# Performance work log

Measured on AMD Instinct MI355X. Metric: run time of the kernel, lower is better.

Reference implementation:

```python
import jax, jax.numpy as jnp
import numpy as np

B, S, D = 16384, 2048, 512

def mish(z):
    # z * tanh(softplus(z))
    return z * jnp.tanh(jax.nn.softplus(z))

def setup_inputs() -> dict:
    key = jax.random.key(0)
    ks = jax.random.split(key, 8)
    sc_d = 1.0 / np.sqrt(D)
    sc_s = 1.0 / np.sqrt(S)
    return {
        "x": jax.random.normal(ks[0], (B, D), jnp.float32),
        "samples": jax.random.normal(ks[1], (S, D), jnp.float32),
        "W1": jax.random.normal(ks[2], (D, D), jnp.float32) * sc_d,
        "b1": jax.random.normal(ks[3], (D,), jnp.float32) * sc_d,
        "W2": jax.random.normal(ks[4], (D, D), jnp.float32) * sc_d,
        "b2": jax.random.normal(ks[5], (D,), jnp.float32) * sc_d,
        "Wn1": jax.random.normal(ks[6], (S, S), jnp.float32) * sc_s,
        "Wn2": jax.random.normal(ks[7], (S, S), jnp.float32) * sc_s,
    }

def reference(x, samples, W1, b1, W2, b2, Wn1, Wn2):
    def dml(t):
        h = mish(t @ W1.T + b1)
        return h @ W2.T + b2

    # forward: x -> dml -> rbf kernel vs dml(samples) -> nystrom MLP
    x_dml = dml(x)            # [B, D]
    sam_new = dml(samples)    # [S, D]

    # fused batched cdist (Euclidean, not squared) + RBF
    d2 = (jnp.sum(x_dml * x_dml, axis=-1, keepdims=True)
          + jnp.sum(sam_new * sam_new, axis=-1)[None, :]
          - 2.0 * (x_dml @ sam_new.T))
    dist = jnp.sqrt(jnp.maximum(d2, 0.0))
    K = jnp.exp(-dist)        # [B, S] == exp(-||xi - sam_j||_2)

    # nystrom MLP (no bias)
    h = mish(K @ Wn1.T)
    return h @ Wn2.T          # [B, S]
```

## Files before the change

kernel.cpp:

```cpp
#include <hip/hip_runtime.h>
#include <cstdint>
#include <cstddef>

#define B_ROWS 16384
#define S_ROWS 2048
#define D_DIM  512

typedef __attribute__((ext_vector_type(8))) short          s16x8;
typedef __attribute__((ext_vector_type(8))) unsigned short u16x8;
typedef __attribute__((ext_vector_type(4))) float          f32x4;

static __device__ __forceinline__ unsigned short f2bf(float f) {
  unsigned int u = __builtin_bit_cast(unsigned int, f);
  u = (u + 0x7FFFu + ((u >> 16) & 1u)) >> 16;
  return (unsigned short)u;
}
static __device__ __forceinline__ float bf2f(unsigned short h) {
  unsigned int u = ((unsigned int)h) << 16;
  return __builtin_bit_cast(float, u);
}
static __device__ __forceinline__ float mish_f(float z) {
  float sp = (z > 20.0f) ? z : log1pf(expf(z));
  return z * tanhf(sp);
}

static __device__ __forceinline__ f32x4 mfma16(s16x8 a, s16x8 b, f32x4 c) {
  return __builtin_amdgcn_mfma_f32_16x16x32_bf16(a, b, c, 0, 0, 0);
}

static __device__ __forceinline__ void gload16(unsigned short* lds_dst,
                                               const unsigned short* g_src) {
  __builtin_amdgcn_global_load_lds(
      (const __attribute__((address_space(1))) unsigned int*)g_src,
      (__attribute__((address_space(3))) unsigned int*)lds_dst,
      16, 0, 0);
}

__global__ void split_kernel(const float* __restrict__ in,
                             unsigned short* __restrict__ hi,
                             unsigned short* __restrict__ lo, int n4) {
  const int stride = gridDim.x * blockDim.x;
  for (int i = blockIdx.x * blockDim.x + threadIdx.x; i < n4; i += stride) {
    const float4 v = ((const float4*)in)[i];
    float f[4] = {v.x, v.y, v.z, v.w};
    unsigned short hh[4], ll[4];
#pragma unroll
    for (int j = 0; j < 4; ++j) {
      hh[j] = f2bf(f[j]);
      ll[j] = f2bf(f[j] - bf2f(hh[j]));
    }
    ((ushort4*)hi)[i] = make_ushort4(hh[0], hh[1], hh[2], hh[3]);
    ((ushort4*)lo)[i] = make_ushort4(ll[0], ll[1], ll[2], ll[3]);
  }
}

__global__ void norm_kernel(const unsigned short* __restrict__ hi,
                            const unsigned short* __restrict__ lo,
                            float* __restrict__ out, int rows) {
  const int gw = (int)((blockIdx.x * blockDim.x + threadIdx.x) >> 6);
  const int l  = threadIdx.x & 63;
  if (gw >= rows) return;
  const size_t base = (size_t)gw * D_DIM + (size_t)l * 8;
  const u16x8 h8 = *(const u16x8*)(hi + base);
  const u16x8 l8 = *(const u16x8*)(lo + base);
  float s = 0.f;
#pragma unroll
  for (int j = 0; j < 8; ++j) {
    float v = bf2f(h8[j]) + bf2f(l8[j]);
    s += v * v;
  }
#pragma unroll
  for (int m = 32; m; m >>= 1) s += __shfl_xor(s, m, 64);
  if (l == 0) out[gw] = s;
}

#define BKT 32

template <int EPI>
__global__ __launch_bounds__(256) void gemm_split(
    const unsigned short* __restrict__ Ahi, const unsigned short* __restrict__ Alo,
    const unsigned short* __restrict__ Bhi, const unsigned short* __restrict__ Blo,
    const float* __restrict__ bias, const float* __restrict__ nrmA,
    const float* __restrict__ nrmB,
    unsigned short* __restrict__ Chi, unsigned short* __restrict__ Clo,
    float* __restrict__ Cf, int M, int N, int K) {
  __shared__ __align__(16) unsigned short lds[4 * 128 * BKT];
  unsigned short* tAh = lds;
  unsigned short* tAl = lds + 128 * BKT;
  unsigned short* tBh = lds + 2 * 128 * BKT;
  unsigned short* tBl = lds + 3 * 128 * BKT;

  const int tid = threadIdx.x;
  const int w = tid >> 6;
  const int l = tid & 63;
  const int nTm = M >> 7;
  const int tm = (int)(blockIdx.x) % nTm;
  const int tn = (int)(blockIdx.x) / nTm;
  const int rowA0 = tm << 7;
  const int rowB0 = tn << 7;

  const int wm = w >> 1, wn = w & 1;
  const int fr = l & 15, fg = l >> 4;

  f32x4 acc[4][4];
#pragma unroll
  for (int i = 0; i < 4; ++i)
#pragma unroll
    for (int j = 0; j < 4; ++j) acc[i][j] = (f32x4){0.f, 0.f, 0.f, 0.f};

  const int srow   = l >> 2;
  const int gchunk = (l & 3) ^ (srow & 3);

  const int nk = K >> 5;
  for (int kt = 0; kt < nk; ++kt) {
    const int k0 = kt << 5;
#pragma unroll
    for (int j = 0; j < 2; ++j) {
      const int rl = w * 32 + j * 16;
      const int gr = rl + srow;
      const size_t ga = (size_t)(rowA0 + gr) * (size_t)K + (size_t)(k0 + gchunk * 8);
      const size_t gb = (size_t)(rowB0 + gr) * (size_t)K + (size_t)(k0 + gchunk * 8);
      gload16(tAh + rl * BKT, Ahi + ga);
      gload16(tAl + rl * BKT, Alo + ga);
      gload16(tBh + rl * BKT, Bhi + gb);
      gload16(tBl + rl * BKT, Blo + gb);
    }
    __syncthreads();

    s16x8 ah[4], al[4], bh[4], bl[4];
#pragma unroll
    for (int mi = 0; mi < 4; ++mi) {
      const int r = wm * 64 + mi * 16 + fr;
      const int c = (fg ^ (r & 3)) << 3;
      ah[mi] = *(const s16x8*)&tAh[r * BKT + c];
      al[mi] = *(const s16x8*)&tAl[r * BKT + c];
    }
#pragma unroll
    for (int ni = 0; ni < 4; ++ni) {
      const int r = wn * 64 + ni * 16 + fr;
      const int c = (fg ^ (r & 3)) << 3;
      bh[ni] = *(const s16x8*)&tBh[r * BKT + c];
      bl[ni] = *(const s16x8*)&tBl[r * BKT + c];
    }
#pragma unroll
    for (int mi = 0; mi < 4; ++mi)
#pragma unroll
      for (int ni = 0; ni < 4; ++ni) {
        acc[mi][ni] = mfma16(al[mi], bh[ni], acc[mi][ni]);
        acc[mi][ni] = mfma16(ah[mi], bl[ni], acc[mi][ni]);
        acc[mi][ni] = mfma16(ah[mi], bh[ni], acc[mi][ni]);
      }
    __syncthreads();
  }

  const int rowBase = rowA0 + wm * 64;
  const int colBase = rowB0 + wn * 64;
#pragma unroll
  for (int mi = 0; mi < 4; ++mi) {
#pragma unroll
    for (int ni = 0; ni < 4; ++ni) {
      const int col = colBase + ni * 16 + fr;
      float badd = 0.f;
      if constexpr (EPI == 0 || EPI == 1) badd = bias[col];
      float nB = 0.f;
      if constexpr (EPI == 2) nB = nrmB[col];
#pragma unroll
      for (int r = 0; r < 4; ++r) {
        const int row = rowBase + mi * 16 + fg * 4 + r;
        float v = acc[mi][ni][r];
        if constexpr (EPI == 0 || EPI == 1) v += badd;
        if constexpr (EPI == 2) {
          float d2 = nrmA[row] + nB - 2.f * v;
          v = expf(-sqrtf(fmaxf(d2, 0.f)));
        }
        if constexpr (EPI == 0 || EPI == 3) v = mish_f(v);
        const size_t o = (size_t)row * (size_t)N + (size_t)col;
        if constexpr (EPI == 4) {
          Cf[o] = v;
        } else {
          unsigned short h = f2bf(v);
          Chi[o] = h;
          Clo[o] = f2bf(v - bf2f(h));
        }
      }
    }
  }
}

template <int EPI>
static void launch_gemm(const unsigned short* Ahi, const unsigned short* Alo,
                        const unsigned short* Bhi, const unsigned short* Blo,
                        const float* bias, const float* nrmA, const float* nrmB,
                        unsigned short* Chi, unsigned short* Clo, float* Cf,
                        int M, int N, int K, hipStream_t stream) {
  dim3 grid((unsigned)((M >> 7) * (N >> 7)));
  gemm_split<EPI><<<grid, dim3(256), 0, stream>>>(Ahi, Alo, Bhi, Blo, bias,
                                                  nrmA, nrmB, Chi, Clo, Cf, M, N, K);
}

static int grid_for(int n4) {
  int g = (n4 + 255) / 256;
  return g > 4096 ? 4096 : g;
}

extern "C" void kernel_launch(void* const* d_in, const int* in_sizes, int n_in,
                              void* d_out, int out_size, void* d_ws, size_t ws_size,
                              hipStream_t stream) {
  const float* x       = (const float*)d_in[0];
  const float* samples = (const float*)d_in[1];
  const float* W1      = (const float*)d_in[2];
  const float* b1      = (const float*)d_in[3];
  const float* W2      = (const float*)d_in[4];
  const float* b2      = (const float*)d_in[5];
  const float* Wn1     = (const float*)d_in[6];
  const float* Wn2     = (const float*)d_in[7];
  float* outF = (float*)d_out;

  if (ws_size < 167845888ull) return;

  char* ob = (char*)d_out;
  unsigned short* xhi  = (unsigned short*)(ob + 0);
  unsigned short* xlo  = (unsigned short*)(ob + 16777216);
  unsigned short* t1hi = (unsigned short*)(ob + 33554432);
  unsigned short* t1lo = (unsigned short*)(ob + 50331648);
  unsigned short* t2hi = (unsigned short*)(ob + 67108864);
  unsigned short* t2lo = (unsigned short*)(ob + 69206016);
  unsigned short* Khi  = (unsigned short*)(ob + 0);
  unsigned short* Klo  = (unsigned short*)(ob + 67108864);

  char* wb = (char*)d_ws;
  unsigned short* hhi  = (unsigned short*)(wb + 0);
  unsigned short* hlo  = (unsigned short*)(wb + 67108864);
  unsigned short* xdhi = (unsigned short*)(wb + 0);
  unsigned short* xdlo = (unsigned short*)(wb + 16777216);
  unsigned short* snhi = (unsigned short*)(wb + 33554432);
  unsigned short* snlo = (unsigned short*)(wb + 35651584);
  unsigned short* samhi= (unsigned short*)(wb + 37748736);
  unsigned short* samlo= (unsigned short*)(wb + 39845888);
  unsigned short* W1hi = (unsigned short*)(wb + 41943040);
  unsigned short* W1lo = (unsigned short*)(wb + 42467328);
  unsigned short* W2hi = (unsigned short*)(wb + 42991616);
  unsigned short* W2lo = (unsigned short*)(wb + 43515904);
  unsigned short* Wn1hi= (unsigned short*)(wb + 134217728);
  unsigned short* Wn1lo= (unsigned short*)(wb + 142606336);
  unsigned short* Wn2hi= (unsigned short*)(wb + 150994944);
  unsigned short* Wn2lo= (unsigned short*)(wb + 159383552);
  float* nx            = (float*)(wb + 167772160);
  float* ns            = (float*)(wb + 167837696);

  const dim3 tpb(256);

  {
    int n4;
    n4 = B_ROWS * D_DIM / 4;
    split_kernel<<<grid_for(n4), tpb, 0, stream>>>(x, xhi, xlo, n4);
    n4 = S_ROWS * D_DIM / 4;
    split_kernel<<<grid_for(n4), tpb, 0, stream>>>(samples, samhi, samlo, n4);
    n4 = D_DIM * D_DIM / 4;
    split_kernel<<<grid_for(n4), tpb, 0, stream>>>(W1, W1hi, W1lo, n4);
    split_kernel<<<grid_for(n4), tpb, 0, stream>>>(W2, W2hi, W2lo, n4);
    n4 = S_ROWS * S_ROWS / 4;
    split_kernel<<<grid_for(n4), tpb, 0, stream>>>(Wn1, Wn1hi, Wn1lo, n4);
    split_kernel<<<grid_for(n4), tpb, 0, stream>>>(Wn2, Wn2hi, Wn2lo, n4);
  }

  launch_gemm<0>(xhi, xlo, W1hi, W1lo, b1, nullptr, nullptr, t1hi, t1lo, nullptr,
                 B_ROWS, D_DIM, D_DIM, stream);
  launch_gemm<1>(t1hi, t1lo, W2hi, W2lo, b2, nullptr, nullptr, xdhi, xdlo, nullptr,
                 B_ROWS, D_DIM, D_DIM, stream);
  launch_gemm<0>(samhi, samlo, W1hi, W1lo, b1, nullptr, nullptr, t2hi, t2lo, nullptr,
                 S_ROWS, D_DIM, D_DIM, stream);
  launch_gemm<1>(t2hi, t2lo, W2hi, W2lo, b2, nullptr, nullptr, snhi, snlo, nullptr,
                 S_ROWS, D_DIM, D_DIM, stream);

  norm_kernel<<<dim3(B_ROWS / 4), tpb, 0, stream>>>(xdhi, xdlo, nx, B_ROWS);
  norm_kernel<<<dim3(S_ROWS / 4), tpb, 0, stream>>>(snhi, snlo, ns, S_ROWS);

  launch_gemm<2>(xdhi, xdlo, snhi, snlo, nullptr, nx, ns, Khi, Klo, nullptr,
                 B_ROWS, S_ROWS, D_DIM, stream);

  launch_gemm<3>(Khi, Klo, Wn1hi, Wn1lo, nullptr, nullptr, nullptr, hhi, hlo, nullptr,
                 B_ROWS, S_ROWS, S_ROWS, stream);

  launch_gemm<4>(hhi, hlo, Wn2hi, Wn2lo, nullptr, nullptr, nullptr, nullptr, nullptr,
                 outF, B_ROWS, S_ROWS, S_ROWS, stream);
}
```

Before: 1.497 ms.

## Interleave hi/lo tiles in LDS with XOR swizzle and XCD-aware block remap

Merges the separate hi and lo LDS tiles into one 128-byte row per matrix row, with an 8-way XOR swizzle so each lane's global load fills either the hi or the lo half. The fragment reads become byte-offset loads where the lo half sits at offset XOR 64. Source and destination pointers are now computed once outside the k-loop. Block indices are remapped so consecutive tiles land on the same XCD, and tile order switches to row-major over N, which is meant to improve L2 reuse. Together these aim to cut LDS bank conflicts, address arithmetic and cross-XCD cache misses, at the cost of more complex index math.

```diff
diff --git a/kernel.cpp b/kernel.cpp
--- a/kernel.cpp
+++ b/kernel.cpp
@@ -74,7 +74,6 @@
   if (l == 0) out[gw] = s;
 }
 
-#define BKT 32
 
 template <int EPI>
 __global__ __launch_bounds__(256) void gemm_split(
@@ -84,18 +83,23 @@
     const float* __restrict__ nrmB,
     unsigned short* __restrict__ Chi, unsigned short* __restrict__ Clo,
     float* __restrict__ Cf, int M, int N, int K) {
-  __shared__ __align__(16) unsigned short lds[4 * 128 * BKT];
-  unsigned short* tAh = lds;
-  unsigned short* tAl = lds + 128 * BKT;
-  unsigned short* tBh = lds + 2 * 128 * BKT;
-  unsigned short* tBl = lds + 3 * 128 * BKT;
+  __shared__ __align__(16) unsigned short lds[2 * 128 * 64];
+  unsigned short* tA = lds;
+  unsigned short* tB = lds + 128 * 64;
 
   const int tid = threadIdx.x;
   const int w = tid >> 6;
   const int l = tid & 63;
-  const int nTm = M >> 7;
-  const int tm = (int)(blockIdx.x) % nTm;
-  const int tn = (int)(blockIdx.x) / nTm;
+
+  const int nwg = (int)gridDim.x;
+  {
+  }
+  const int q8 = nwg >> 3, r8 = nwg & 7;
+  const int xcd = (int)blockIdx.x & 7, boff = (int)blockIdx.x >> 3;
+  const int swz = (xcd < r8 ? xcd * (q8 + 1) : r8 * (q8 + 1) + (xcd - r8) * q8) + boff;
+  const int nTn = N >> 7;
+  const int tm = swz / nTn;
+  const int tn = swz - tm * nTn;
   const int rowA0 = tm << 7;
   const int rowB0 = tn << 7;
 
@@ -108,39 +112,52 @@
 #pragma unroll
     for (int j = 0; j < 4; ++j) acc[i][j] = (f32x4){0.f, 0.f, 0.f, 0.f};
 
-  const int srow   = l >> 2;
-  const int gchunk = (l & 3) ^ (srow & 3);
+  const int pos   = l & 7;
+  const int rsub  = (l >> 3) & 7;
+  const int c     = pos ^ rsub;
+  const bool isHi = (c < 4);
+  const int celem = (c & 3) << 3;
+
+  const unsigned short* srcA[4];
+  const unsigned short* srcB[4];
+  unsigned short* dstA[4];
+  unsigned short* dstB[4];
+#pragma unroll
+  for (int j = 0; j < 4; ++j) {
+    const int rl = w * 32 + j * 8;
+    const int gr = rl + (l >> 3);
+    srcA[j] = (isHi ? Ahi : Alo) + (size_t)(rowA0 + gr) * (size_t)K + celem;
+    srcB[j] = (isHi ? Bhi : Blo) + (size_t)(rowB0 + gr) * (size_t)K + celem;
+    dstA[j] = tA + rl * 64;
+    dstB[j] = tB + rl * 64;
+  }
+
+  const int pbyte = (fg ^ (fr & 7)) << 4;
+  const char* tAc = (const char*)tA;
+  const char* tBc = (const char*)tB;
 
   const int nk = K >> 5;
   for (int kt = 0; kt < nk; ++kt) {
     const int k0 = kt << 5;
 #pragma unroll
-    for (int j = 0; j < 2; ++j) {
-      const int rl = w * 32 + j * 16;
-      const int gr = rl + srow;
-      const size_t ga = (size_t)(rowA0 + gr) * (size_t)K + (size_t)(k0 + gchunk * 8);
-      const size_t gb = (size_t)(rowB0 + gr) * (size_t)K + (size_t)(k0 + gchunk * 8);
-      gload16(tAh + rl * BKT, Ahi + ga);
-      gload16(tAl + rl * BKT, Alo + ga);
-      gload16(tBh + rl * BKT, Bhi + gb);
-      gload16(tBl + rl * BKT, Blo + gb);
+    for (int j = 0; j < 4; ++j) {
+      gload16(dstA[j], srcA[j] + k0);
+      gload16(dstB[j], srcB[j] + k0);
     }
     __syncthreads();
 
     s16x8 ah[4], al[4], bh[4], bl[4];
 #pragma unroll
     for (int mi = 0; mi < 4; ++mi) {
-      const int r = wm * 64 + mi * 16 + fr;
-      const int c = (fg ^ (r & 3)) << 3;
-      ah[mi] = *(const s16x8*)&tAh[r * BKT + c];
-      al[mi] = *(const s16x8*)&tAl[r * BKT + c];
+      const int base = ((wm << 6) + (mi << 4) + fr) << 7;
+      ah[mi] = *(const s16x8*)(tAc + (base + pbyte));
+      al[mi] = *(const s16x8*)(tAc + ((base + pbyte) ^ 64));
     }
 #pragma unroll
     for (int ni = 0; ni < 4; ++ni) {
-      const int r = wn * 64 + ni * 16 + fr;
-      const int c = (fg ^ (r & 3)) << 3;
-      bh[ni] = *(const s16x8*)&tBh[r * BKT + c];
-      bl[ni] = *(const s16x8*)&tBl[r * BKT + c];
+      const int base = ((wn << 6) + (ni << 4) + fr) << 7;
+      bh[ni] = *(const s16x8*)(tBc + (base + pbyte));
+      bl[ni] = *(const s16x8*)(tBc + ((base + pbyte) ^ 64));
     }
 #pragma unroll
     for (int mi = 0; mi < 4; ++mi)
```

Measured after the change: 1.475 ms. Within noise of the previous version (-1.5%).

## Rewrite split-bf16 GEMM as 256x256 tile, 4-stage pipelined, XCD-swizzled kernel

Applied to the files above, without the earlier changes.

Replaces the 128x128, 256-thread GEMM with a 256x256 tile over 512 threads. It streams the three split-bf16 products (hi*hi, hi*lo, lo*hi) as consecutive K passes through a 4-slot LDS ring, with explicit vmcnt waits and raw barriers so global loads overlap MFMA work. It also adds XCD-aware block remapping, a new LDS swizzle, and s_setprio around the MFMA block. The goal is to hide global-load latency, raise data reuse per tile and improve L2 locality, at the cost of a large register footprint (8x4 accumulators), 128KB of LDS per block, and hand-counted waitcnt logic that is fragile.

```diff
diff --git a/kernel.cpp b/kernel.cpp
--- a/kernel.cpp
+++ b/kernel.cpp
@@ -74,89 +74,117 @@
   if (l == 0) out[gw] = s;
 }
 
-#define BKT 32
-
 template <int EPI>
-__global__ __launch_bounds__(256) void gemm_split(
+__global__ __launch_bounds__(512, 2) void gemm8(
     const unsigned short* __restrict__ Ahi, const unsigned short* __restrict__ Alo,
     const unsigned short* __restrict__ Bhi, const unsigned short* __restrict__ Blo,
     const float* __restrict__ bias, const float* __restrict__ nrmA,
     const float* __restrict__ nrmB,
     unsigned short* __restrict__ Chi, unsigned short* __restrict__ Clo,
     float* __restrict__ Cf, int M, int N, int K) {
-  __shared__ __align__(16) unsigned short lds[4 * 128 * BKT];
-  unsigned short* tAh = lds;
-  unsigned short* tAl = lds + 128 * BKT;
-  unsigned short* tBh = lds + 2 * 128 * BKT;
-  unsigned short* tBl = lds + 3 * 128 * BKT;
+  __shared__ __align__(16) unsigned short lds[4 * 16384];
 
   const int tid = threadIdx.x;
-  const int w = tid >> 6;
-  const int l = tid & 63;
-  const int nTm = M >> 7;
-  const int tm = (int)(blockIdx.x) % nTm;
-  const int tn = (int)(blockIdx.x) / nTm;
-  const int rowA0 = tm << 7;
-  const int rowB0 = tn << 7;
-
-  const int wm = w >> 1, wn = w & 1;
+  const int w = tid >> 6, l = tid & 63;
+  const int wm = w >> 2, wn = w & 3;
   const int fr = l & 15, fg = l >> 4;
 
-  f32x4 acc[4][4];
-#pragma unroll
-  for (int i = 0; i < 4; ++i)
+  const int nwg = (int)gridDim.x;
+  const int q8 = nwg >> 3, r8 = nwg & 7;
+  const int xcd = (int)blockIdx.x & 7, boff = (int)blockIdx.x >> 3;
+  const int swz = (xcd < r8 ? xcd * (q8 + 1) : r8 * (q8 + 1) + (xcd - r8) * q8) + boff;
+  const int nTn = N >> 8;
+  const int tm = swz / nTn, tn = swz - tm * nTn;
+  const int rowA0 = tm << 8, rowB0 = tn << 8;
+
+  int rE[2], kcE[2];
+#pragma unroll
+  for (int e = 0; e < 2; ++e) {
+    const int d = tid + e * 512;
+    const int pr = d >> 3;
+    const int c8 = (d & 7) ^ (pr & 7);
+    rE[e]  = (pr << 1) | (c8 >> 2);
+    kcE[e] = (c8 & 3) << 3;
+  }
+  size_t gofA0 = (size_t)(rowA0 + rE[0]) * (size_t)K + kcE[0];
+  size_t gofA1 = (size_t)(rowA0 + rE[1]) * (size_t)K + kcE[1];
+  size_t gofB0 = (size_t)(rowB0 + rE[0]) * (size_t)K + kcE[0];
+  size_t gofB1 = (size_t)(rowB0 + rE[1]) * (size_t)K + kcE[1];
+  const int wof = w << 9;
+
+  int iss_slot = 0, iss_k = 0, iss_pass = 0;
+  const unsigned short* pA = Ahi;
+  const unsigned short* pB = Bhi;
+
+#define ISSUE_UNIT()                                                     \
+  do {                                                                   \
+    unsigned short* sb = lds + (iss_slot << 14);                         \
+    gload16(sb + wof,          pA + iss_k + gofA0);                      \
+    gload16(sb + 4096 + wof,   pA + iss_k + gofA1);                      \
+    gload16(sb + 8192 + wof,   pB + iss_k + gofB0);                      \
+    gload16(sb + 12288 + wof,  pB + iss_k + gofB1);                      \
+    iss_slot = (iss_slot + 1) & 3;                                       \
+    iss_k += 32;                                                         \
+    if (iss_k == K) {                                                    \
+      iss_k = 0; ++iss_pass;                                             \
+      pA = (iss_pass == 2) ? Alo : Ahi;                                  \
+      pB = (iss_pass == 1) ? Blo : Bhi;                                  \
+    }                                                                    \
+  } while (0)
+
+  const int frh = fr >> 1;
+  const int p = (((fr & 1) << 2) | fg) ^ (frh & 7);
+  const int aab = ((wm << 6) + frh) * 128 + p * 16;
+  const int bbb = 16384 + ((wn << 5) + frh) * 128 + p * 16;
+
+  f32x4 acc[8][4];
+#pragma unroll
+  for (int i = 0; i < 8; ++i)
 #pragma unroll
     for (int j = 0; j < 4; ++j) acc[i][j] = (f32x4){0.f, 0.f, 0.f, 0.f};
 
-  const int srow   = l >> 2;
-  const int gchunk = (l & 3) ^ (srow & 3);
-
-  const int nk = K >> 5;
-  for (int kt = 0; kt < nk; ++kt) {
-    const int k0 = kt << 5;
-#pragma unroll
-    for (int j = 0; j < 2; ++j) {
-      const int rl = w * 32 + j * 16;
-      const int gr = rl + srow;
-      const size_t ga = (size_t)(rowA0 + gr) * (size_t)K + (size_t)(k0 + gchunk * 8);
-      const size_t gb = (size_t)(rowB0 + gr) * (size_t)K + (size_t)(k0 + gchunk * 8);
-      gload16(tAh + rl * BKT, Ahi + ga);
-      gload16(tAl + rl * BKT, Alo + ga);
-      gload16(tBh + rl * BKT, Bhi + gb);
-      gload16(tBl + rl * BKT, Blo + gb);
+  const int nu = 3 * (K >> 5);
+
+  ISSUE_UNIT();
+  ISSUE_UNIT();
+  ISSUE_UNIT();
+
+  for (int u = 0; u < nu; ++u) {
+    __builtin_amdgcn_s_barrier();
+    if (u + 3 < nu) {
+      ISSUE_UNIT();
+      asm volatile("s_waitcnt vmcnt(12)" ::: "memory");
+    } else if (u == nu - 3) {
+      asm volatile("s_waitcnt vmcnt(8)" ::: "memory");
+    } else if (u == nu - 2) {
+      asm volatile("s_waitcnt vmcnt(4)" ::: "memory");
+    } else {
+      asm volatile("s_waitcnt vmcnt(0)" ::: "memory");
     }
-    __syncthreads();
-
-    s16x8 ah[4], al[4], bh[4], bl[4];
-#pragma unroll
-    for (int mi = 0; mi < 4; ++mi) {
-      const int r = wm * 64 + mi * 16 + fr;
-      const int c = (fg ^ (r & 3)) << 3;
-      ah[mi] = *(const s16x8*)&tAh[r * BKT + c];
-      al[mi] = *(const s16x8*)&tAl[r * BKT + c];
-    }
-#pragma unroll
-    for (int ni = 0; ni < 4; ++ni) {
-      const int r = wn * 64 + ni * 16 + fr;
-      const int c = (fg ^ (r & 3)) << 3;
-      bh[ni] = *(const s16x8*)&tBh[r * BKT + c];
-      bl[ni] = *(const s16x8*)&tBl[r * BKT + c];
-    }
-#pragma unroll
-    for (int mi = 0; mi < 4; ++mi)
-#pragma unroll
-      for (int ni = 0; ni < 4; ++ni) {
-        acc[mi][ni] = mfma16(al[mi], bh[ni], acc[mi][ni]);
-        acc[mi][ni] = mfma16(ah[mi], bl[ni], acc[mi][ni]);
-        acc[mi][ni] = mfma16(ah[mi], bh[ni], acc[mi][ni]);
-      }
-    __syncthreads();
-  }
-
-  const int rowBase = rowA0 + wm * 64;
-  const int colBase = rowB0 + wn * 64;
-#pragma unroll
-  for (int mi = 0; mi < 4; ++mi) {
+    __builtin_amdgcn_s_barrier();
+
+    const char* sc = (const char*)lds + ((size_t)(u & 3) << 15);
+    s16x8 af[8], bf[4];
+#pragma unroll
+    for (int mi = 0; mi < 8; ++mi) af[mi] = *(const s16x8*)(sc + aab + (mi << 10));
+#pragma unroll
+    for (int ni = 0; ni < 4; ++ni) bf[ni] = *(const s16x8*)(sc + bbb + (ni << 10));
+
+    __builtin_amdgcn_s_setprio(1);
+#pragma unroll
+    for (int mi = 0; mi < 8; ++mi)
+#pragma unroll
+      for (int ni = 0; ni < 4; ++ni)
+        acc[mi][ni] = mfma16(af[mi], bf[ni], acc[mi][ni]);
+    __builtin_amdgcn_s_setprio(0);
+    asm volatile("s_waitcnt lgkmcnt(0)" ::: "memory");
+  }
+#undef ISSUE_UNIT
+
+  const int rowBase = rowA0 + (wm << 7);
+  const int colBase = rowB0 + (wn << 6);
+#pragma unroll
+  for (int mi = 0; mi < 8; ++mi) {
 #pragma unroll
     for (int ni = 0; ni < 4; ++ni) {
       const int col = colBase + ni * 16 + fr;
@@ -193,9 +221,9 @@
                         const float* bias, const float* nrmA, const float* nrmB,
                         unsigned short* Chi, unsigned short* Clo, float* Cf,
                         int M, int N, int K, hipStream_t stream) {
-  dim3 grid((unsigned)((M >> 7) * (N >> 7)));
-  gemm_split<EPI><<<grid, dim3(256), 0, stream>>>(Ahi, Alo, Bhi, Blo, bias,
-                                                  nrmA, nrmB, Chi, Clo, Cf, M, N, K);
+  dim3 grid((unsigned)((M >> 8) * (N >> 8)));
+  gemm8<EPI><<<grid, dim3(512), 0, stream>>>(Ahi, Alo, Bhi, Blo, bias,
+                                             nrmA, nrmB, Chi, Clo, Cf, M, N, K);
 }
 
 static int grid_for(int n4) {
```

Result: no change. 1.521 ms (+1.6%).
